# Kernel tuning notes

Measured on AMD Instinct MI355X. Metric: run time of the kernel, lower is better.

The kernel has to match this reference:

```python
import jax, jax.numpy as jnp
import numpy as np

B, H, C, HID, WIN, K = 8, 64, 128, 512, 4, 3
L = H * H

def _conv(x, w, groups, pad):
    return jax.lax.conv_general_dilated(
        x, w, (1, 1), [(pad, pad), (pad, pad)],
        dimension_numbers=('NCHW', 'OIHW', 'NCHW'), feature_group_count=groups)

def _ln(x, g, b):
    m = x.mean(-1, keepdims=True)
    v = ((x - m) ** 2).mean(-1, keepdims=True)
    return (x - m) * jax.lax.rsqrt(v + 1e-5) * g + b

def _gelu(x):
    return jax.nn.gelu(x, approximate=False)  # torch nn.GELU default = erf

def setup_inputs() -> dict:
    key = jax.random.key(0)
    ks = jax.random.split(key, 16)
    n = lambda i, sh: jax.random.normal(ks[i], sh, jnp.float32) * 0.02
    return dict(
        x=jax.random.normal(ks[0], (B, L, C), jnp.float32),
        ln1_g=jnp.ones((C,), jnp.float32), ln1_b=jnp.zeros((C,), jnp.float32),
        conv1_w=n(1, (WIN * C, C, K, K)),
        w_down=n(2, (WIN, C)), b_down=jnp.zeros((WIN,), jnp.float32),
        w1=n(3, (4 * WIN, WIN)), b1=jnp.zeros((4 * WIN,), jnp.float32),
        w2=n(4, (WIN, 4 * WIN)), b2=jnp.zeros((WIN,), jnp.float32),
        w_gk=n(5, (C, WIN * C)), b_gk=jnp.zeros((C,), jnp.float32),
        w_fus=n(6, (C, (WIN + 1) * C)), b_fus=jnp.zeros((C,), jnp.float32),
        ln2_g=jnp.ones((C,), jnp.float32), ln2_b=jnp.zeros((C,), jnp.float32),
        lin1_w=n(7, (HID, C)), lin1_b=jnp.zeros((HID,), jnp.float32),
        dw_w=n(8, (HID, 1, K, K)), dw_b=jnp.zeros((HID,), jnp.float32),
        lin2_w=n(9, (C, HID)), lin2_b=jnp.zeros((C,), jnp.float32),
    )

def _kernel_attn(x, conv1_w, w_down, b_down, w1, b1, w2, b2, w_gk, b_gk, w_fus, b_fus):
    ws = H // 2  # window grid is 2x2 since win_num=4
    xw = x.reshape(B, 2, ws, 2, ws, C).transpose(0, 1, 3, 5, 2, 4).reshape(B, WIN * C, ws, ws)
    wc = _conv(xw, conv1_w, WIN, 1)
    # WinKernel_Reweight (SE over windows)
    pooled = wc.mean((2, 3)).reshape(B, WIN, C)
    y = jnp.einsum('bgc,gc->bg', pooled, w_down) + b_down
    y = _gelu(y @ w1.T + b1)
    wgt = jax.nn.sigmoid(y @ w2.T + b2)
    k0 = conv1_w.reshape(WIN, C, C, K, K)
    kern = wgt[:, :, None, None, None, None] * k0[None]
    k_in = kern.transpose(0, 2, 1, 3, 4, 5).reshape(B * C, WIN * C, K, K)
    gk = jnp.einsum('om,nmij->noij', w_gk, k_in) + b_gk[None, :, None, None]
    kernels = jnp.concatenate([kern, gk.reshape(B, 1, C, C, K, K)], axis=1)
    kernels = kernels.reshape(B * (WIN + 1) * C, C, K, K)
    # per-sample dynamic grouped conv over full-resolution image
    ximg = x.reshape(B, H, H, C).transpose(0, 3, 1, 2)     # [B, C, H, W]
    xrep = jnp.tile(ximg, (1, WIN + 1, 1, 1)).reshape(1, B * (WIN + 1) * C, H, H)
    out = _conv(xrep, kernels, B * (WIN + 1), 1).reshape(B, (WIN + 1) * C, H, H)
    out = jnp.einsum('oc,bchw->bohw', w_fus, out) + b_fus[None, :, None, None]
    return out.transpose(0, 2, 3, 1).reshape(B, L, C)

def _leff(x, lin1_w, lin1_b, dw_w, dw_b, lin2_w, lin2_b):
    h = _gelu(x @ lin1_w.T + lin1_b)                       # [B, L, HID]
    h = h.reshape(B, H, H, HID).transpose(0, 3, 1, 2)
    h = _gelu(_conv(h, dw_w, HID, 1) + dw_b[None, :, None, None])  # depthwise 3x3
    h = h.transpose(0, 2, 3, 1).reshape(B, L, HID)
    return h @ lin2_w.T + lin2_b

def reference(x, ln1_g, ln1_b, conv1_w, w_down, b_down, w1, b1, w2, b2,
              w_gk, b_gk, w_fus, b_fus, ln2_g, ln2_b,
              lin1_w, lin1_b, dw_w, dw_b, lin2_w, lin2_b):
    x = x + _kernel_attn(_ln(x, ln1_g, ln1_b), conv1_w, w_down, b_down,
                         w1, b1, w2, b2, w_gk, b_gk, w_fus, b_fus)
    x = x + _leff(_ln(x, ln2_g, ln2_b), lin1_w, lin1_b, dw_w, dw_b, lin2_w, lin2_b)
    return x
```

## Files before the change

kernel.cpp:

```cpp
#include <hip/hip_runtime.h>
#include <math.h>

#define NB   8
#define HH   64
#define NC   128
#define NHID 512
#define NL   4096

typedef __attribute__((ext_vector_type(4))) float f32x4;
typedef __attribute__((ext_vector_type(8))) __bf16 bf16x8;

__device__ __forceinline__ float gelu_f(float v) {
  return 0.5f * v * (1.f + erff(v * 0.70710678118654752f));
}
__device__ __forceinline__ float sigmoid_f(float v) {
  return 1.f / (1.f + expf(-v));
}
__device__ __forceinline__ unsigned short f2bf(float f) {
  unsigned int u = __builtin_bit_cast(unsigned int, f);
  unsigned int r = (u + 0x7FFFu + ((u >> 16) & 1u)) >> 16;
  return (unsigned short)r;
}
__device__ __forceinline__ float bf2f(unsigned short h) {
  return __builtin_bit_cast(float, ((unsigned int)h) << 16);
}
__device__ __forceinline__ float bflo(unsigned int w) {
  return __builtin_bit_cast(float, w << 16);
}
__device__ __forceinline__ float bfhi(unsigned int w) {
  return __builtin_bit_cast(float, w & 0xFFFF0000u);
}
__device__ __forceinline__ void gld16(const void* g, void* l) {
  __builtin_amdgcn_global_load_lds(
      (const __attribute__((address_space(1))) unsigned int*)g,
      (__attribute__((address_space(3))) unsigned int*)l, 16, 0, 0);
}

__device__ __forceinline__ void bf16x8_store(const float4& a, const float4& b, void* dst) {
  unsigned int p0 = (unsigned int)f2bf(a.x) | ((unsigned int)f2bf(a.y) << 16);
  unsigned int p1 = (unsigned int)f2bf(a.z) | ((unsigned int)f2bf(a.w) << 16);
  unsigned int p2 = (unsigned int)f2bf(b.x) | ((unsigned int)f2bf(b.y) << 16);
  unsigned int p3 = (unsigned int)f2bf(b.z) | ((unsigned int)f2bf(b.w) << 16);
  *(uint4*)dst = make_uint4(p0, p1, p2, p3);
}

__global__ __launch_bounds__(256) void head_kernel(const float* __restrict__ x,
    const float* __restrict__ ln1_g, const float* __restrict__ ln1_b,
    unsigned short* __restrict__ xln,
    const float* __restrict__ lin1_w, const float* __restrict__ lin2_w,
    const float* __restrict__ w_gk, const float* __restrict__ w_fus,
    const float* __restrict__ dw_w, const float* __restrict__ conv1_w,
    unsigned short* __restrict__ w1o, unsigned short* __restrict__ w2o,
    unsigned short* __restrict__ wgko, unsigned short* __restrict__ wf1o,
    unsigned short* __restrict__ wf2o, float* __restrict__ dwt,
    float* __restrict__ sfus,
    unsigned short* __restrict__ ctp, unsigned short* __restrict__ ctq) {
  int gblk = blockIdx.x, tid = threadIdx.x;
  if (gblk < 8192) {
    int wv = tid >> 6, l = tid & 63;
    int row = gblk * 4 + wv;
    const float2 v = *(const float2*)(x + (size_t)row * NC + l * 2);
    float s = v.x + v.y, ss = v.x * v.x + v.y * v.y;
#pragma unroll
    for (int off = 32; off > 0; off >>= 1) {
      s  += __shfl_down(s, off);
      ss += __shfl_down(ss, off);
    }
    s = __shfl(s, 0); ss = __shfl(ss, 0);
    float mean = s * (1.f / NC);
    float rstd = rsqrtf(ss * (1.f / NC) - mean * mean + 1e-5f);
    const float2 gg = *(const float2*)(ln1_g + l * 2);
    const float2 bv = *(const float2*)(ln1_b + l * 2);
    float o0 = (v.x - mean) * rstd * gg.x + bv.x;
    float o1 = (v.y - mean) * rstd * gg.y + bv.y;
    unsigned int pk = (unsigned int)f2bf(o0) | ((unsigned int)f2bf(o1) << 16);
    *(unsigned int*)((char*)xln + (size_t)row * 256 + ((l >> 2) << 4) + (l & 3) * 4) = pk;
    return;
  }
  if (gblk < 8347) {
    int blk = gblk - 8192;
    if (blk < 32) {
      int idx = blk * 256 + tid;
      int n = idx >> 4, c16 = idx & 15;
      const float4 a = *(const float4*)(lin1_w + (size_t)n * 128 + c16 * 8);
      const float4 b = *(const float4*)(lin1_w + (size_t)n * 128 + c16 * 8 + 4);
      bf16x8_store(a, b, (char*)w1o + (size_t)n * 256 + ((c16 ^ (n & 7)) << 4));
    } else if (blk < 64) {
      int idx = (blk - 32) * 256 + tid;
      int kt = idx >> 11, c = (idx >> 4) & 127, c16 = idx & 15;
      const float* s = lin2_w + (size_t)c * NHID + kt * 128 + c16 * 8;
      const float4 a = *(const float4*)(s);
      const float4 b = *(const float4*)(s + 4);
      bf16x8_store(a, b, (char*)w2o + (size_t)(kt * 128 + c) * 256 + ((c16 ^ (c & 7)) << 4));
    } else if (blk < 96) {
      int idx = (blk - 64) * 256 + tid;
      int row = idx >> 4, c16 = idx & 15;
      int w = row >> 7, q = row & 127;
      const float* s = w_gk + (size_t)q * 512 + w * 128 + c16 * 8;
      const float4 a = *(const float4*)(s);
      const float4 b = *(const float4*)(s + 4);
      bf16x8_store(a, b, (char*)wgko + (size_t)row * 256 + ((c16 ^ (row & 7)) << 4));
    } else if (blk < 136) {
      int idx = (blk - 96) * 256 + tid;
      if (idx < 8192) {
        int row = idx >> 4, c16 = idx & 15;
        int w = row >> 7, o = row & 127;
        const float* s = w_fus + (size_t)o * 640 + w * 128 + c16 * 8;
        const float4 a = *(const float4*)(s);
        const float4 b = *(const float4*)(s + 4);
        bf16x8_store(a, b, (char*)wf1o + (size_t)row * 256 + ((c16 ^ (row & 7)) << 4));
      } else if (idx < 10240) {
        int i2 = idx - 8192;
        int row = i2 >> 4, c16 = i2 & 15;
        const float* s = w_fus + (size_t)row * 640 + 512 + c16 * 8;
        const float4 a = *(const float4*)(s);
        const float4 b = *(const float4*)(s + 4);
        bf16x8_store(a, b, (char*)wf2o + (size_t)row * 256 + ((c16 ^ (row & 7)) << 4));
      }
    } else if (blk < 154) {
      int idx = (blk - 136) * 256 + tid;
      if (idx < 4608) {
        int p = idx / 1152, rem = idx - p * 1152;
        int tap = rem >> 7, c = rem & 127;
        dwt[idx] = dw_w[(size_t)(p * 128 + c) * 9 + tap];
      }
    } else {
      if (tid < 128) {
        float s = 0;
        for (int p = 0; p < 128; ++p) s += w_fus[(size_t)tid * 640 + 512 + p];
        sfus[tid] = s;
      }
    }
    return;
  }
  {
    int oc = (gblk - 8347) * 2 + (tid >> 7);
    int w = oc >> 7, c = oc & 127;
    int t = tid & 127;
    float v[9];
#pragma unroll
    for (int j = 0; j < 9; ++j) v[j] = conv1_w[(size_t)oc * 1152 + t * 9 + j];
#pragma unroll
    for (int j = 0; j < 9; ++j) {
      unsigned short bv = f2bf(v[j]);
      size_t prow = (size_t)(w * 9 + j) * 128 + c;
      *(unsigned short*)((char*)ctp + prow * 256 + ((((t >> 3) ^ (c & 7)) << 4) + (t & 7) * 2)) = bv;
      size_t qrow = (size_t)(w * 9 + j) * 128 + t;
      *(unsigned short*)((char*)ctq + qrow * 256 + ((((c >> 3) ^ (t & 7)) << 4) + (c & 7) * 2)) = bv;
    }
  }
}

__global__ __launch_bounds__(128) void rs_kernel(const unsigned short* __restrict__ xln,
    float* __restrict__ RS) {
  int blk = blockIdx.x;
  int r = blk & 31, bw = blk >> 5;
  int win = bw & 3, b = bw >> 2;
  int hw = win >> 1, wn = win & 1;
  int cin = threadIdx.x;
  const unsigned short* base = xln + (((size_t)(b * 64 + hw * 32 + r)) * 64 + wn * 32) * NC + cin;
  float s = 0;
#pragma unroll
  for (int c = 0; c < 32; ++c) s += bf2f(base[(size_t)c * NC]);
  RS[(size_t)blk * 128 + cin] = s;
}

__global__ __launch_bounds__(256) void gemmGT_kernel(const unsigned short* __restrict__ Wgk,
    const unsigned short* __restrict__ CTP, const float* __restrict__ w_down,
    unsigned short* __restrict__ Gbf, float* __restrict__ U,
    const unsigned short* __restrict__ xln, const float* __restrict__ RS,
    float* __restrict__ T) {
  int gblk = blockIdx.x;
  int tid = threadIdx.x;
  if (gblk >= 36) {
    if (tid >= 128) return;
    int bw = gblk - 36;
    int win = bw & 3, b = bw >> 2;
    int hw = win >> 1, wn = win & 1;
    int cin = tid;
    const unsigned short* base = xln + (((size_t)(b * 64 + hw * 32)) * 64 + wn * 32) * NC + cin;
    float A = 0;
#pragma unroll
    for (int r = 0; r < 32; ++r) A += RS[(size_t)(bw * 32 + r) * 128 + cin];
    float r0  = RS[(size_t)(bw * 32) * 128 + cin];
    float r31 = RS[(size_t)(bw * 32 + 31) * 128 + cin];
    float c0 = 0, c31 = 0;
#pragma unroll
    for (int r = 0; r < 32; ++r) {
      c0  += bf2f(base[((size_t)r * 64) * NC]);
      c31 += bf2f(base[((size_t)r * 64 + 31) * NC]);
    }
    float x00 = bf2f(base[0]);
    float x0c = bf2f(base[(size_t)31 * NC]);
    float xr0 = bf2f(base[((size_t)31 * 64) * NC]);
    float xrc = bf2f(base[((size_t)31 * 64 + 31) * NC]);
    float* t = T + ((size_t)bw * 128 + cin) * 9;
    t[0] = A - r31 - c31 + xrc;
    t[1] = A - r31;
    t[2] = A - r31 - c0 + xr0;
    t[3] = A - c31;
    t[4] = A;
    t[5] = A - c0;
    t[6] = A - r0 - c31 + x0c;
    t[7] = A - r0;
    t[8] = A - r0 - c0 + x00;
    return;
  }
  __shared__ uint4 LA[2048];
  __shared__ uint4 LB[2048];
  int bx = gblk;
  int w = bx / 9;
  int wv = tid >> 6, l = tid & 63;
  const char* ga = (const char*)Wgk + (size_t)w * 32768;
  const char* gb = (const char*)CTP + (size_t)bx * 32768;
  for (int i = wv; i < 32; i += 4) gld16(ga + (i << 10) + l * 16, (char*)LA + (i << 10));
  for (int i = wv; i < 32; i += 4) gld16(gb + (i << 10) + l * 16, (char*)LB + (i << 10));
  __syncthreads();
  const f32x4 zero = {0.f, 0.f, 0.f, 0.f};
  f32x4 acc[2][8];
#pragma unroll
  for (int mt = 0; mt < 2; ++mt)
#pragma unroll
    for (int nt = 0; nt < 8; ++nt) acc[mt][nt] = zero;
  bf16x8 af[2][4];
#pragma unroll
  for (int mt = 0; mt < 2; ++mt) {
    int r = wv * 16 + mt * 64 + (l & 15);
#pragma unroll
    for (int ks = 0; ks < 4; ++ks) {
      int c16 = ks * 4 + (l >> 4);
      af[mt][ks] = *(const bf16x8*)((const char*)LA + r * 256 + ((c16 ^ (r & 7)) << 4));
    }
  }
#pragma unroll
  for (int nt = 0; nt < 8; ++nt) {
    int n = nt * 16 + (l & 15);
    bf16x8 bq[4];
#pragma unroll
    for (int ks = 0; ks < 4; ++ks) {
      int c16 = ks * 4 + (l >> 4);
      bq[ks] = *(const bf16x8*)((const char*)LB + n * 256 + ((c16 ^ (n & 7)) << 4));
    }
#pragma unroll
    for (int ks = 0; ks < 4; ++ks)
#pragma unroll
      for (int mt = 0; mt < 2; ++mt)
        acc[mt][nt] = __builtin_amdgcn_mfma_f32_16x16x32_bf16(af[mt][ks], bq[ks], acc[mt][nt], 0, 0, 0);
  }
  char* gout = (char*)Gbf + (size_t)bx * 32768;
#pragma unroll
  for (int mt = 0; mt < 2; ++mt)
#pragma unroll
    for (int nt = 0; nt < 8; ++nt) {
      int p = nt * 16 + (l & 15);
#pragma unroll
      for (int r2 = 0; r2 < 4; ++r2) {
        int q = wv * 16 + mt * 64 + (l >> 4) * 4 + r2;
        *(unsigned short*)(gout + q * 256 + ((((p >> 3) ^ (q & 7)) << 4) + (p & 7) * 2)) =
            f2bf(acc[mt][nt][r2]);
      }
    }
  if (tid < 128) {
    int cin = tid;
    int hi = cin >> 3, lo = (cin & 7) * 2;
    float s = 0;
    for (int cout = 0; cout < 128; ++cout) {
      unsigned short bv = *(const unsigned short*)((const char*)LB + cout * 256 +
                                                   (((hi ^ (cout & 7)) << 4) + lo));
      s += w_down[w * 128 + cout] * bf2f(bv);
    }
    U[(size_t)bx * 128 + cin] = s;
  }
}

__global__ __launch_bounds__(256) void gemmAWse_kernel(const unsigned short* __restrict__ Wf1,
    const unsigned short* __restrict__ CTQ, const unsigned short* __restrict__ Wf2,
    const unsigned short* __restrict__ Gbf, float* __restrict__ AW,
    const float* __restrict__ T, const float* __restrict__ U,
    const float* __restrict__ b_down, const float* __restrict__ w1,
    const float* __restrict__ b1, const float* __restrict__ w2,
    const float* __restrict__ b2, float* __restrict__ wgt) {
  __shared__ uint4 LA[2048];
  __shared__ uint4 LB[2048];
  int gblk = blockIdx.x;
  int tid = threadIdx.x;
  if (gblk == 36) {
    float* ydot = (float*)LA;
    int pair = tid >> 3, sub = tid & 7;
    int g = pair & 3;
    float acc = 0;
    for (int k = 0; k < 16; ++k) {
      int cin = sub * 16 + k;
      const float* tp = T + ((size_t)pair * 128 + cin) * 9;
#pragma unroll
      for (int ij = 0; ij < 9; ++ij)
        acc += U[(size_t)(g * 9 + ij) * 128 + cin] * tp[ij];
    }
#pragma unroll
    for (int off = 4; off > 0; off >>= 1) acc += __shfl_down(acc, off);
    if (sub == 0) ydot[pair] = acc;
    __syncthreads();
    if (tid < NB) {
      int b = tid;
      float y[4];
#pragma unroll
      for (int gg = 0; gg < 4; ++gg) y[gg] = ydot[b * 4 + gg] * (1.f / 1024.f) + b_down[gg];
      float y1[16];
#pragma unroll
      for (int i = 0; i < 16; ++i) {
        float a = b1[i];
#pragma unroll
        for (int gg = 0; gg < 4; ++gg) a += y[gg] * w1[i * 4 + gg];
        y1[i] = gelu_f(a);
      }
#pragma unroll
      for (int gg = 0; gg < 4; ++gg) {
        float a = b2[gg];
#pragma unroll
        for (int i = 0; i < 16; ++i) a += y1[i] * w2[gg * 16 + i];
        wgt[b * 4 + gg] = sigmoid_f(a);
      }
    }
    return;
  }
  int bx = gblk;
  int w = bx / 9;
  int wv = tid >> 6, l = tid & 63;
  const f32x4 zero = {0.f, 0.f, 0.f, 0.f};
  f32x4 acc[2][8];
#pragma unroll
  for (int mt = 0; mt < 2; ++mt)
#pragma unroll
    for (int nt = 0; nt < 8; ++nt) acc[mt][nt] = zero;
  for (int ph = 0; ph < 2; ++ph) {
    if (ph) __syncthreads();
    const char* ga = ph ? (const char*)Wf2 : (const char*)Wf1 + (size_t)w * 32768;
    const char* gb = ph ? (const char*)Gbf + (size_t)bx * 32768
                        : (const char*)CTQ + (size_t)bx * 32768;
    for (int i = wv; i < 32; i += 4) gld16(ga + (i << 10) + l * 16, (char*)LA + (i << 10));
    for (int i = wv; i < 32; i += 4) gld16(gb + (i << 10) + l * 16, (char*)LB + (i << 10));
    __syncthreads();
    bf16x8 af[2][4];
#pragma unroll
    for (int mt = 0; mt < 2; ++mt) {
      int r = wv * 16 + mt * 64 + (l & 15);
#pragma unroll
      for (int ks = 0; ks < 4; ++ks) {
        int c16 = ks * 4 + (l >> 4);
        af[mt][ks] = *(const bf16x8*)((const char*)LA + r * 256 + ((c16 ^ (r & 7)) << 4));
      }
    }
#pragma unroll
    for (int nt = 0; nt < 8; ++nt) {
      int n = nt * 16 + (l & 15);
      bf16x8 bq[4];
#pragma unroll
      for (int ks = 0; ks < 4; ++ks) {
        int c16 = ks * 4 + (l >> 4);
        bq[ks] = *(const bf16x8*)((const char*)LB + n * 256 + ((c16 ^ (n & 7)) << 4));
      }
#pragma unroll
      for (int ks = 0; ks < 4; ++ks)
#pragma unroll
        for (int mt = 0; mt < 2; ++mt)
          acc[mt][nt] = __builtin_amdgcn_mfma_f32_16x16x32_bf16(af[mt][ks], bq[ks], acc[mt][nt], 0, 0, 0);
    }
  }
  float* aout = AW + (size_t)bx * 16384;
#pragma unroll
  for (int mt = 0; mt < 2; ++mt)
#pragma unroll
    for (int nt = 0; nt < 8; ++nt) {
      int q = nt * 16 + (l & 15);
#pragma unroll
      for (int r2 = 0; r2 < 4; ++r2) {
        int o = wv * 16 + mt * 64 + (l >> 4) * 4 + r2;
        aout[(size_t)o * 128 + q] = acc[mt][nt][r2];
      }
    }
}

__global__ __launch_bounds__(128) void m_kernel(const float* __restrict__ AW,
    const float* __restrict__ wgt, const float* __restrict__ sfus,
    const float* __restrict__ b_gk, unsigned short* __restrict__ Mb) {
  int blk = blockIdx.x;
  int b = blk >> 7;
  int o = blk & 127;
  int q = threadIdx.x;
  float a3 = sfus[o] * b_gk[q];
  float acc[9];
#pragma unroll
  for (int ij = 0; ij < 9; ++ij) acc[ij] = a3;
#pragma unroll
  for (int w = 0; w < 4; ++w) {
    float wv = wgt[b * 4 + w];
#pragma unroll
    for (int ij = 0; ij < 9; ++ij)
      acc[ij] += wv * AW[(((size_t)(w * 9 + ij) * 128 + o) * 128) + q];
  }
  int qswz = (q & 7) | (((q >> 3) ^ (o & 7)) << 3);
#pragma unroll
  for (int ij = 0; ij < 9; ++ij)
    Mb[(((size_t)(b * 9 + ij) * NC + o) * NC) + qswz] = f2bf(acc[ij]);
}

__global__ __launch_bounds__(256) void conv_kernel(const float* __restrict__ x0,
    const unsigned short* __restrict__ xln, const unsigned short* __restrict__ Mb,
    const float* __restrict__ b_fus, const float* __restrict__ ln2g,
    const float* __restrict__ ln2b, unsigned short* __restrict__ xatt,
    unsigned short* __restrict__ xln2) {
  __shared__ uint4 XT[1600];
  __shared__ uint4 MT[2048];
  int bx = blockIdx.x;
  int b = bx >> 6, tile = bx & 63;
  int by = (tile >> 3) * 8, bxc = (tile & 7) * 8;
  int tid = threadIdx.x, wv = tid >> 6, l = tid & 63;
  for (int i = tid; i < 1600; i += 256) {
    int cell = i >> 4, c16 = i & 15;
    int pr = cell / 10, pc = cell - pr * 10;
    int gy = by + pr - 1, gx = bxc + pc - 1;
    uint4 v = make_uint4(0, 0, 0, 0);
    if ((unsigned)gy < 64u && (unsigned)gx < 64u)
      v = *(const uint4*)(xln + (((size_t)b * NL + gy * 64 + gx) * NC + c16 * 8));
    *(uint4*)((char*)XT + cell * 256 + ((c16 ^ (cell & 7)) << 4)) = v;
  }
  const char* mg = (const char*)Mb + (size_t)b * 9 * 32768;
  for (int i = wv; i < 32; i += 4) gld16(mg + (i << 10) + l * 16, (char*)MT + (i << 10));
  __syncthreads();

  const f32x4 zero = {0.f, 0.f, 0.f, 0.f};
  f32x4 acc[8];
#pragma unroll
  for (int nt = 0; nt < 8; ++nt) acc[nt] = zero;

  int sp = wv * 16 + (l & 15);
  int srow = sp >> 3, scol = sp & 7;

  for (int ij = 0; ij < 9; ++ij) {
    int di = ij / 3, dj = ij - di * 3;
    int cell = (srow + di) * 10 + scol + dj;
    bf16x8 af[4];
#pragma unroll
    for (int ks = 0; ks < 4; ++ks) {
      int c16 = ks * 4 + (l >> 4);
      af[ks] = *(const bf16x8*)((const char*)XT + cell * 256 + ((c16 ^ (cell & 7)) << 4));
    }
#pragma unroll
    for (int nt = 0; nt < 8; ++nt) {
      int oc = nt * 16 + (l & 15);
      bf16x8 bq[4];
#pragma unroll
      for (int ks = 0; ks < 4; ++ks) {
        int c16 = ks * 4 + (l >> 4);
        bq[ks] = *(const bf16x8*)((const char*)MT + oc * 256 + ((c16 ^ (oc & 7)) << 4));
      }
#pragma unroll
      for (int ks = 0; ks < 4; ++ks)
        acc[nt] = __builtin_amdgcn_mfma_f32_16x16x32_bf16(af[ks], bq[ks], acc[nt], 0, 0, 0);
    }
    __syncthreads();
    if (ij < 8) {
      const char* mg2 = mg + (size_t)(ij + 1) * 32768;
      for (int i = wv; i < 32; i += 4) gld16(mg2 + (i << 10) + l * 16, (char*)MT + (i << 10));
    }
    __syncthreads();
  }
  float s[4] = {0, 0, 0, 0}, ss2[4] = {0, 0, 0, 0};
  float vals[8][4];
#pragma unroll
  for (int nt = 0; nt < 8; ++nt) {
    int oc = nt * 16 + (l & 15);
    float bfv = b_fus[oc];
#pragma unroll
    for (int r2 = 0; r2 < 4; ++r2) {
      int sp2 = wv * 16 + (l >> 4) * 4 + r2;
      int gy = by + (sp2 >> 3), gx = bxc + (sp2 & 7);
      size_t gi = ((size_t)b * NL + gy * 64 + gx) * NC + oc;
      float v = x0[gi] + acc[nt][r2] + bfv;
      xatt[gi] = f2bf(v);
      vals[nt][r2] = v;
      s[r2] += v;
      ss2[r2] += v * v;
    }
  }
#pragma unroll
  for (int r2 = 0; r2 < 4; ++r2) {
#pragma unroll
    for (int off = 1; off < 16; off <<= 1) {
      s[r2]   += __shfl_xor(s[r2], off);
      ss2[r2] += __shfl_xor(ss2[r2], off);
    }
  }
  float mean[4], rstd[4];
#pragma unroll
  for (int r2 = 0; r2 < 4; ++r2) {
    mean[r2] = s[r2] * (1.f / 128.f);
    rstd[r2] = rsqrtf(ss2[r2] * (1.f / 128.f) - mean[r2] * mean[r2] + 1e-5f);
  }
#pragma unroll
  for (int nt = 0; nt < 8; ++nt) {
    int oc = nt * 16 + (l & 15);
    float gv = ln2g[oc], bv = ln2b[oc];
    int cc16 = oc >> 3, cby = (oc & 7) * 2;
#pragma unroll
    for (int r2 = 0; r2 < 4; ++r2) {
      int sp2 = wv * 16 + (l >> 4) * 4 + r2;
      int gy = by + (sp2 >> 3), gx = bxc + (sp2 & 7);
      size_t rowg = (size_t)b * NL + gy * 64 + gx;
      float o = (vals[nt][r2] - mean[r2]) * rstd[r2] * gv + bv;
      *(unsigned short*)((char*)xln2 + rowg * 256 + (((size_t)(cc16 ^ (int)(rowg & 7))) << 4) + cby) = f2bf(o);
    }
  }
}

__global__ __launch_bounds__(256) void lin1_kernel(const unsigned short* __restrict__ xa,
    const unsigned short* __restrict__ wb, const float* __restrict__ bias,
    unsigned short* __restrict__ h1p0, unsigned short* __restrict__ h1p123) {
  __shared__ uint4 XA[1024];
  __shared__ uint4 XB[2048];
  size_t rb = (size_t)blockIdx.x * 64;
  int tid = threadIdx.x, wv = tid >> 6, l = tid & 63;
  const char* ga = (const char*)xa + rb * 256;
  for (int i = wv; i < 16; i += 4) gld16(ga + (i << 10) + l * 16, (char*)XA + (i << 10));
  for (int i = wv; i < 32; i += 4) gld16((const char*)wb + (i << 10) + l * 16, (char*)XB + (i << 10));
  __syncthreads();
  int r = wv * 16 + (l & 15);
  bf16x8 af[4];
#pragma unroll
  for (int ks = 0; ks < 4; ++ks) {
    int c16 = ks * 4 + (l >> 4);
    af[ks] = *(const bf16x8*)((const char*)XA + r * 256 + ((c16 ^ (r & 7)) << 4));
  }
  const f32x4 zero = {0.f, 0.f, 0.f, 0.f};
  for (int cb = 0; cb < 4; ++cb) {
    f32x4 acc[8];
#pragma unroll
    for (int nt = 0; nt < 8; ++nt) acc[nt] = zero;
#pragma unroll
    for (int nt = 0; nt < 8; ++nt) {
      int n = nt * 16 + (l & 15);
      bf16x8 bq[4];
#pragma unroll
      for (int ks = 0; ks < 4; ++ks) {
        int c16 = ks * 4 + (l >> 4);
        bq[ks] = *(const bf16x8*)((const char*)XB + n * 256 + ((c16 ^ (n & 7)) << 4));
      }
#pragma unroll
      for (int ks = 0; ks < 4; ++ks)
        acc[nt] = __builtin_amdgcn_mfma_f32_16x16x32_bf16(af[ks], bq[ks], acc[nt], 0, 0, 0);
    }
    if (cb < 3) {
      __syncthreads();
      const char* gb = (const char*)wb + (size_t)(cb + 1) * 32768;
      for (int i = wv; i < 32; i += 4) gld16(gb + (i << 10) + l * 16, (char*)XB + (i << 10));
    }
    unsigned short* hp = (cb == 0) ? h1p0 : h1p123 + (size_t)(cb - 1) * 4194304;
#pragma unroll
    for (int nt = 0; nt < 8; ++nt) {
      int n = nt * 16 + (l & 15);
      float bsv = bias[cb * 128 + n];
#pragma unroll
      for (int r2 = 0; r2 < 4; ++r2) {
        size_t row = rb + wv * 16 + (l >> 4) * 4 + r2;
        hp[row * 128 + n] = f2bf(gelu_f(acc[nt][r2] + bsv));
      }
    }
    if (cb < 3) __syncthreads();
  }
}

__global__ __launch_bounds__(256) void dw_kernel(const unsigned short* __restrict__ h1p0,
    const unsigned short* __restrict__ h1p123, const float* __restrict__ dwt,
    const float* __restrict__ dw_b, unsigned short* __restrict__ h2p0,
    unsigned short* __restrict__ h2p123) {
  __shared__ unsigned char HT[6 * 64 * 128];
  __shared__ float wsm[9][64];
  int bx = blockIdx.x;
  int cp = bx >> 7;
  int rem = bx & 127;
  int bimg = rem >> 4, ys = rem & 15;
  int p = cp >> 1, chh = cp & 1;
  int y0 = ys * 4;
  int tid = threadIdx.x, wv = tid >> 6, l = tid & 63;
  const unsigned short* h1p = p ? h1p123 + (size_t)(p - 1) * 4194304 : h1p0;
  unsigned short* h2p = p ? h2p123 + (size_t)(p - 1) * 4194304 : h2p0;
  size_t ibase = (size_t)bimg * 4096;
  for (int i = tid; i < 576; i += 256)
    wsm[0][i] = dwt[(size_t)p * 1152 + (i >> 6) * 128 + chh * 64 + (i & 63)];
#pragma unroll
  for (int it = 0; it < 12; ++it) {
    int cb = it * 4 + wv;
    int row = cb >> 3, colblk = cb & 7;
    int yy = y0 - 1 + row;
    int ldsbase = (row * 64 + colblk * 8) * 128;
    if ((unsigned)yy < 64u) {
      const char* src = (const char*)h1p +
          (ibase + (size_t)yy * 64 + colblk * 8 + (l >> 3)) * 256 + chh * 128 + (l & 7) * 16;
      gld16(src, (char*)HT + ldsbase);
    } else {
      *(uint4*)((char*)HT + ldsbase + l * 16) = make_uint4(0, 0, 0, 0);
    }
  }
  int grp = tid >> 3, c8 = tid & 7;
  int ch0 = p * 128 + chh * 64 + c8 * 8;
  const float4 bs0 = *(const float4*)(dw_b + ch0);
  const float4 bs1 = *(const float4*)(dw_b + ch0 + 4);
  __syncthreads();

#pragma unroll
  for (int r = 0; r < 4; ++r) {
#pragma unroll
    for (int cc = 0; cc < 2; ++cc) {
      int col = grp * 2 + cc;
      float acw[8];
      acw[0] = bs0.x; acw[1] = bs0.y; acw[2] = bs0.z; acw[3] = bs0.w;
      acw[4] = bs1.x; acw[5] = bs1.y; acw[6] = bs1.z; acw[7] = bs1.w;
#pragma unroll
      for (int dy = 0; dy < 3; ++dy) {
#pragma unroll
        for (int dx = 0; dx < 3; ++dx) {
          int xc = col + dx - 1;
          if ((unsigned)xc < 64u) {
            const uint4 u = *(const uint4*)((const char*)HT +
                (((r + dy) * 64 + xc) * 128) + c8 * 16);
            const float4 wa  = *(const float4*)(&wsm[dy * 3 + dx][c8 * 8]);
            const float4 wb2 = *(const float4*)(&wsm[dy * 3 + dx][c8 * 8 + 4]);
            acw[0] += wa.x * bflo(u.x);  acw[1] += wa.y * bfhi(u.x);
            acw[2] += wa.z * bflo(u.y);  acw[3] += wa.w * bfhi(u.y);
            acw[4] += wb2.x * bflo(u.z); acw[5] += wb2.y * bfhi(u.z);
            acw[6] += wb2.z * bflo(u.w); acw[7] += wb2.w * bfhi(u.w);
          }
        }
      }
      size_t sidx = ibase + (size_t)(y0 + r) * 64 + col;
      int c16o = chh * 8 + c8;
      unsigned int o0 = (unsigned int)f2bf(gelu_f(acw[0])) | ((unsigned int)f2bf(gelu_f(acw[1])) << 16);
      unsigned int o1 = (unsigned int)f2bf(gelu_f(acw[2])) | ((unsigned int)f2bf(gelu_f(acw[3])) << 16);
      unsigned int o2 = (unsigned int)f2bf(gelu_f(acw[4])) | ((unsigned int)f2bf(gelu_f(acw[5])) << 16);
      unsigned int o3 = (unsigned int)f2bf(gelu_f(acw[6])) | ((unsigned int)f2bf(gelu_f(acw[7])) << 16);
      *(uint4*)(h2p + sidx * 128 + ((c16o ^ (int)(sidx & 7)) << 3)) = make_uint4(o0, o1, o2, o3);
    }
  }
}

__global__ __launch_bounds__(256) void lin2_kernel(const unsigned short* __restrict__ h2p0,
    const unsigned short* __restrict__ h2p123, const unsigned short* __restrict__ wb,
    const float* __restrict__ bias, const unsigned short* __restrict__ xres,
    float* __restrict__ out) {
  __shared__ uint4 XA[1024];
  __shared__ uint4 XB[2048];
  size_t rb = (size_t)blockIdx.x * 64;
  int tid = threadIdx.x, wv = tid >> 6, l = tid & 63;
  const f32x4 zero = {0.f, 0.f, 0.f, 0.f};
  f32x4 acc[8];
#pragma unroll
  for (int nt = 0; nt < 8; ++nt) acc[nt] = zero;
  int r = wv * 16 + (l & 15);
  for (int kt = 0; kt < 4; ++kt) {
    if (kt) __syncthreads();
    const unsigned short* hp = (kt == 0) ? h2p0 : h2p123 + (size_t)(kt - 1) * 4194304;
    const char* ga = (const char*)hp + rb * 256;
    const char* gb = (const char*)wb + (size_t)kt * 32768;
    for (int i = wv; i < 16; i += 4) gld16(ga + (i << 10) + l * 16, (char*)XA + (i << 10));
    for (int i = wv; i < 32; i += 4) gld16(gb + (i << 10) + l * 16, (char*)XB + (i << 10));
    __syncthreads();
    bf16x8 af[4];
#pragma unroll
    for (int ks = 0; ks < 4; ++ks) {
      int c16 = ks * 4 + (l >> 4);
      af[ks] = *(const bf16x8*)((const char*)XA + r * 256 + ((c16 ^ (r & 7)) << 4));
    }
#pragma unroll
    for (int nt = 0; nt < 8; ++nt) {
      int n = nt * 16 + (l & 15);
      bf16x8 bq[4];
#pragma unroll
      for (int ks = 0; ks < 4; ++ks) {
        int c16 = ks * 4 + (l >> 4);
        bq[ks] = *(const bf16x8*)((const char*)XB + n * 256 + ((c16 ^ (n & 7)) << 4));
      }
#pragma unroll
      for (int ks = 0; ks < 4; ++ks)
        acc[nt] = __builtin_amdgcn_mfma_f32_16x16x32_bf16(af[ks], bq[ks], acc[nt], 0, 0, 0);
    }
  }
#pragma unroll
  for (int nt = 0; nt < 8; ++nt) {
    int n = nt * 16 + (l & 15);
    float bsv = bias[n];
#pragma unroll
    for (int r2 = 0; r2 < 4; ++r2) {
      size_t row = rb + wv * 16 + (l >> 4) * 4 + r2;
      size_t gi = row * NC + n;
      out[gi] = bf2f(xres[gi]) + acc[nt][r2] + bsv;
    }
  }
}

extern "C" void kernel_launch(void* const* d_in, const int* in_sizes, int n_in,
                              void* d_out, int out_size, void* d_ws, size_t ws_size,
                              hipStream_t stream) {
  (void)in_sizes; (void)n_in; (void)out_size; (void)ws_size;
  const float* x       = (const float*)d_in[0];
  const float* ln1_g   = (const float*)d_in[1];
  const float* ln1_b   = (const float*)d_in[2];
  const float* conv1_w = (const float*)d_in[3];
  const float* w_down  = (const float*)d_in[4];
  const float* b_down  = (const float*)d_in[5];
  const float* w1      = (const float*)d_in[6];
  const float* b1      = (const float*)d_in[7];
  const float* w2      = (const float*)d_in[8];
  const float* b2      = (const float*)d_in[9];
  const float* w_gk    = (const float*)d_in[10];
  const float* b_gk    = (const float*)d_in[11];
  const float* w_fus   = (const float*)d_in[12];
  const float* b_fus   = (const float*)d_in[13];
  const float* ln2_g   = (const float*)d_in[14];
  const float* ln2_b   = (const float*)d_in[15];
  const float* lin1_w  = (const float*)d_in[16];
  const float* lin1_b  = (const float*)d_in[17];
  const float* dw_w    = (const float*)d_in[18];
  const float* dw_b    = (const float*)d_in[19];
  const float* lin2_w  = (const float*)d_in[20];
  const float* lin2_b  = (const float*)d_in[21];
  float* out = (float*)d_out;
  char* ws = (char*)d_ws;

  unsigned short* xatt_bf = (unsigned short*)(ws);
  float*          Tb      = (float*)(ws + 16777216);
  float*          wgtb    = (float*)(ws + 16924672);
  float*          sfus    = (float*)(ws + 16925184);
  float*          dwt     = (float*)(ws + 16925696);
  unsigned short* Wgk_bf  = (unsigned short*)(ws + 16944128);
  unsigned short* Wf1_bf  = (unsigned short*)(ws + 17075200);
  unsigned short* Wf2_bf  = (unsigned short*)(ws + 17206272);
  unsigned short* w1_bf   = (unsigned short*)(ws + 17239040);
  unsigned short* w2_bf   = (unsigned short*)(ws + 17370112);
  unsigned short* M_bf    = (unsigned short*)(ws + 17501184);
  unsigned short* xln_bf  = (unsigned short*)(ws + 19860480);
  unsigned short* xln2_bf = (unsigned short*)(ws + 28249088);
  unsigned short* h1p123  = (unsigned short*)(ws + 36637696);
  unsigned short* h2p123  = (unsigned short*)(ws + 61803520);
  char* sc = ws + 28249088;
  float*          RSb     = (float*)(sc);
  float*          Ub      = (float*)(sc + 524288);
  unsigned short* CTP_bf  = (unsigned short*)(sc + 542720);
  unsigned short* CTQ_bf  = (unsigned short*)(sc + 1722368);
  unsigned short* G_bf    = (unsigned short*)(sc + 2902016);
  float*          AWb     = (float*)(sc + 4081664);

  head_kernel<<<8603, 256, 0, stream>>>(x, ln1_g, ln1_b, xln_bf,
                                        lin1_w, lin2_w, w_gk, w_fus, dw_w, conv1_w,
                                        w1_bf, w2_bf, Wgk_bf, Wf1_bf, Wf2_bf, dwt, sfus,
                                        CTP_bf, CTQ_bf);
  rs_kernel<<<1024, 128, 0, stream>>>(xln_bf, RSb);
  gemmGT_kernel<<<68, 256, 0, stream>>>(Wgk_bf, CTP_bf, w_down, G_bf, Ub,
                                        xln_bf, RSb, Tb);
  gemmAWse_kernel<<<37, 256, 0, stream>>>(Wf1_bf, CTQ_bf, Wf2_bf, G_bf, AWb,
                                          Tb, Ub, b_down, w1, b1, w2, b2, wgtb);
  m_kernel<<<1024, 128, 0, stream>>>(AWb, wgtb, sfus, b_gk, M_bf);
  conv_kernel<<<512, 256, 0, stream>>>(x, xln_bf, M_bf, b_fus, ln2_g, ln2_b, xatt_bf, xln2_bf);
  lin1_kernel<<<512, 256, 0, stream>>>(xln2_bf, w1_bf, lin1_b, xln_bf , h1p123);
  dw_kernel<<<1024, 256, 0, stream>>>(xln_bf , h1p123, dwt, dw_b,
                                      xln2_bf , h2p123);
  lin2_kernel<<<512, 256, 0, stream>>>(xln2_bf , h2p123, w2_bf, lin2_b, xatt_bf, out);
}
```

Baseline: 149.8 us.

## Retile conv waves as 2x2 grid and split depthwise halo load

The fused conv kernel now gives each wave 32 spatial rows by 64 output channels instead of 16 rows by all 128 channels, so every B-fragment load from LDS feeds two MFMAs. Because each wave now sees only half the channels, the LayerNorm statistics are combined across wave pairs through shared memory, which adds an extra barrier. The depthwise kernel issues only the first 8 of 12 halo row loads before computing output rows 0-1, then loads the remaining rows and computes rows 2-3, to overlap global loads with compute. The early barrier before rows 0-1 does not obviously wait for the async loads of the last four halo rows before rows 2-3 read them, so correctness depends on how gld16 behaves.

```diff
diff --git a/kernel.cpp b/kernel.cpp
--- a/kernel.cpp
+++ b/kernel.cpp
@@ -415,6 +415,7 @@
   int b = bx >> 6, tile = bx & 63;
   int by = (tile >> 3) * 8, bxc = (tile & 7) * 8;
   int tid = threadIdx.x, wv = tid >> 6, l = tid & 63;
+  int sh = wv >> 1, oh = wv & 1;
   for (int i = tid; i < 1600; i += 256) {
     int cell = i >> 4, c16 = i & 15;
     int pr = cell / 10, pc = cell - pr * 10;
@@ -429,25 +430,28 @@
   __syncthreads();
 
   const f32x4 zero = {0.f, 0.f, 0.f, 0.f};
-  f32x4 acc[8];
-#pragma unroll
-  for (int nt = 0; nt < 8; ++nt) acc[nt] = zero;
-
-  int sp = wv * 16 + (l & 15);
-  int srow = sp >> 3, scol = sp & 7;
+  f32x4 acc[2][4];
+#pragma unroll
+  for (int mt = 0; mt < 2; ++mt)
+#pragma unroll
+    for (int nt = 0; nt < 4; ++nt) acc[mt][nt] = zero;
 
   for (int ij = 0; ij < 9; ++ij) {
     int di = ij / 3, dj = ij - di * 3;
-    int cell = (srow + di) * 10 + scol + dj;
-    bf16x8 af[4];
-#pragma unroll
-    for (int ks = 0; ks < 4; ++ks) {
-      int c16 = ks * 4 + (l >> 4);
-      af[ks] = *(const bf16x8*)((const char*)XT + cell * 256 + ((c16 ^ (cell & 7)) << 4));
-    }
-#pragma unroll
-    for (int nt = 0; nt < 8; ++nt) {
-      int oc = nt * 16 + (l & 15);
+    bf16x8 af[2][4];
+#pragma unroll
+    for (int mt = 0; mt < 2; ++mt) {
+      int sp = sh * 32 + mt * 16 + (l & 15);
+      int cell = ((sp >> 3) + di) * 10 + (sp & 7) + dj;
+#pragma unroll
+      for (int ks = 0; ks < 4; ++ks) {
+        int c16 = ks * 4 + (l >> 4);
+        af[mt][ks] = *(const bf16x8*)((const char*)XT + cell * 256 + ((c16 ^ (cell & 7)) << 4));
+      }
+    }
+#pragma unroll
+    for (int nt = 0; nt < 4; ++nt) {
+      int oc = oh * 64 + nt * 16 + (l & 15);
       bf16x8 bq[4];
 #pragma unroll
       for (int ks = 0; ks < 4; ++ks) {
@@ -456,7 +460,9 @@
       }
 #pragma unroll
       for (int ks = 0; ks < 4; ++ks)
-        acc[nt] = __builtin_amdgcn_mfma_f32_16x16x32_bf16(af[ks], bq[ks], acc[nt], 0, 0, 0);
+#pragma unroll
+        for (int mt = 0; mt < 2; ++mt)
+          acc[mt][nt] = __builtin_amdgcn_mfma_f32_16x16x32_bf16(af[mt][ks], bq[ks], acc[mt][nt], 0, 0, 0);
     }
     __syncthreads();
     if (ij < 8) {
@@ -465,52 +471,82 @@
     }
     __syncthreads();
   }
-  float s[4] = {0, 0, 0, 0}, ss2[4] = {0, 0, 0, 0};
-  float vals[8][4];
-#pragma unroll
-  for (int nt = 0; nt < 8; ++nt) {
-    int oc = nt * 16 + (l & 15);
-    float bfv = b_fus[oc];
+  float* pS  = (float*)XT;
+  float* pSS = (float*)XT + 128;
+  float s[2][4], ss2[2][4];
+  float vals[2][4][4];
+#pragma unroll
+  for (int mt = 0; mt < 2; ++mt)
+#pragma unroll
+    for (int r2 = 0; r2 < 4; ++r2) { s[mt][r2] = 0.f; ss2[mt][r2] = 0.f; }
+#pragma unroll
+  for (int mt = 0; mt < 2; ++mt)
+#pragma unroll
+    for (int nt = 0; nt < 4; ++nt) {
+      int oc = oh * 64 + nt * 16 + (l & 15);
+      float bfv = b_fus[oc];
+#pragma unroll
+      for (int r2 = 0; r2 < 4; ++r2) {
+        int sp2 = sh * 32 + mt * 16 + (l >> 4) * 4 + r2;
+        int gy = by + (sp2 >> 3), gx = bxc + (sp2 & 7);
+        size_t gi = ((size_t)b * NL + gy * 64 + gx) * NC + oc;
+        float v = x0[gi] + acc[mt][nt][r2] + bfv;
+        xatt[gi] = f2bf(v);
+        vals[mt][nt][r2] = v;
+        s[mt][r2] += v;
+        ss2[mt][r2] += v * v;
+      }
+    }
+#pragma unroll
+  for (int mt = 0; mt < 2; ++mt)
 #pragma unroll
     for (int r2 = 0; r2 < 4; ++r2) {
-      int sp2 = wv * 16 + (l >> 4) * 4 + r2;
-      int gy = by + (sp2 >> 3), gx = bxc + (sp2 & 7);
-      size_t gi = ((size_t)b * NL + gy * 64 + gx) * NC + oc;
-      float v = x0[gi] + acc[nt][r2] + bfv;
-      xatt[gi] = f2bf(v);
-      vals[nt][r2] = v;
-      s[r2] += v;
-      ss2[r2] += v * v;
-    }
-  }
-#pragma unroll
-  for (int r2 = 0; r2 < 4; ++r2) {
-#pragma unroll
-    for (int off = 1; off < 16; off <<= 1) {
-      s[r2]   += __shfl_xor(s[r2], off);
-      ss2[r2] += __shfl_xor(ss2[r2], off);
-    }
-  }
-  float mean[4], rstd[4];
-#pragma unroll
-  for (int r2 = 0; r2 < 4; ++r2) {
-    mean[r2] = s[r2] * (1.f / 128.f);
-    rstd[r2] = rsqrtf(ss2[r2] * (1.f / 128.f) - mean[r2] * mean[r2] + 1e-5f);
-  }
-#pragma unroll
-  for (int nt = 0; nt < 8; ++nt) {
-    int oc = nt * 16 + (l & 15);
-    float gv = ln2g[oc], bv = ln2b[oc];
-    int cc16 = oc >> 3, cby = (oc & 7) * 2;
+#pragma unroll
+      for (int off = 1; off < 16; off <<= 1) {
+        s[mt][r2]   += __shfl_xor(s[mt][r2], off);
+        ss2[mt][r2] += __shfl_xor(ss2[mt][r2], off);
+      }
+    }
+  if ((l & 15) == 0) {
+    int g = l >> 4;
+#pragma unroll
+    for (int mt = 0; mt < 2; ++mt)
+#pragma unroll
+      for (int r2 = 0; r2 < 4; ++r2) {
+        int row = sh * 32 + mt * 16 + g * 4 + r2;
+        pS[oh * 64 + row]  = s[mt][r2];
+        pSS[oh * 64 + row] = ss2[mt][r2];
+      }
+  }
+  __syncthreads();
+  float mean[2][4], rstd[2][4];
+#pragma unroll
+  for (int mt = 0; mt < 2; ++mt)
 #pragma unroll
     for (int r2 = 0; r2 < 4; ++r2) {
-      int sp2 = wv * 16 + (l >> 4) * 4 + r2;
-      int gy = by + (sp2 >> 3), gx = bxc + (sp2 & 7);
-      size_t rowg = (size_t)b * NL + gy * 64 + gx;
-      float o = (vals[nt][r2] - mean[r2]) * rstd[r2] * gv + bv;
-      *(unsigned short*)((char*)xln2 + rowg * 256 + (((size_t)(cc16 ^ (int)(rowg & 7))) << 4) + cby) = f2bf(o);
-    }
-  }
+      int row = sh * 32 + mt * 16 + (l >> 4) * 4 + r2;
+      float S  = pS[row] + pS[64 + row];
+      float SS = pSS[row] + pSS[64 + row];
+      float m = S * (1.f / 128.f);
+      mean[mt][r2] = m;
+      rstd[mt][r2] = rsqrtf(SS * (1.f / 128.f) - m * m + 1e-5f);
+    }
+#pragma unroll
+  for (int mt = 0; mt < 2; ++mt)
+#pragma unroll
+    for (int nt = 0; nt < 4; ++nt) {
+      int oc = oh * 64 + nt * 16 + (l & 15);
+      float gv = ln2g[oc], bv = ln2b[oc];
+      int cc16 = oc >> 3, cby = (oc & 7) * 2;
+#pragma unroll
+      for (int r2 = 0; r2 < 4; ++r2) {
+        int sp2 = sh * 32 + mt * 16 + (l >> 4) * 4 + r2;
+        int gy = by + (sp2 >> 3), gx = bxc + (sp2 & 7);
+        size_t rowg = (size_t)b * NL + gy * 64 + gx;
+        float o = (vals[mt][nt][r2] - mean[mt][r2]) * rstd[mt][r2] * gv + bv;
+        *(unsigned short*)((char*)xln2 + rowg * 256 + (((size_t)(cc16 ^ (int)(rowg & 7))) << 4) + cby) = f2bf(o);
+      }
+    }
 }
 
 __global__ __launch_bounds__(256) void lin1_kernel(const unsigned short* __restrict__ xa,
@@ -588,7 +624,7 @@
   for (int i = tid; i < 576; i += 256)
     wsm[0][i] = dwt[(size_t)p * 1152 + (i >> 6) * 128 + chh * 64 + (i & 63)];
 #pragma unroll
-  for (int it = 0; it < 12; ++it) {
+  for (int it = 0; it < 8; ++it) {
     int cb = it * 4 + wv;
     int row = cb >> 3, colblk = cb & 7;
     int yy = y0 - 1 + row;
@@ -606,41 +642,61 @@
   const float4 bs0 = *(const float4*)(dw_b + ch0);
   const float4 bs1 = *(const float4*)(dw_b + ch0 + 4);
   __syncthreads();
-
-#pragma unroll
-  for (int r = 0; r < 4; ++r) {
-#pragma unroll
-    for (int cc = 0; cc < 2; ++cc) {
-      int col = grp * 2 + cc;
-      float acw[8];
-      acw[0] = bs0.x; acw[1] = bs0.y; acw[2] = bs0.z; acw[3] = bs0.w;
-      acw[4] = bs1.x; acw[5] = bs1.y; acw[6] = bs1.z; acw[7] = bs1.w;
-#pragma unroll
-      for (int dy = 0; dy < 3; ++dy) {
-#pragma unroll
-        for (int dx = 0; dx < 3; ++dx) {
-          int xc = col + dx - 1;
-          if ((unsigned)xc < 64u) {
-            const uint4 u = *(const uint4*)((const char*)HT +
-                (((r + dy) * 64 + xc) * 128) + c8 * 16);
-            const float4 wa  = *(const float4*)(&wsm[dy * 3 + dx][c8 * 8]);
-            const float4 wb2 = *(const float4*)(&wsm[dy * 3 + dx][c8 * 8 + 4]);
-            acw[0] += wa.x * bflo(u.x);  acw[1] += wa.y * bfhi(u.x);
-            acw[2] += wa.z * bflo(u.y);  acw[3] += wa.w * bfhi(u.y);
-            acw[4] += wb2.x * bflo(u.z); acw[5] += wb2.y * bfhi(u.z);
-            acw[6] += wb2.z * bflo(u.w); acw[7] += wb2.w * bfhi(u.w);
-          }
-        }
-      }
-      size_t sidx = ibase + (size_t)(y0 + r) * 64 + col;
-      int c16o = chh * 8 + c8;
-      unsigned int o0 = (unsigned int)f2bf(gelu_f(acw[0])) | ((unsigned int)f2bf(gelu_f(acw[1])) << 16);
-      unsigned int o1 = (unsigned int)f2bf(gelu_f(acw[2])) | ((unsigned int)f2bf(gelu_f(acw[3])) << 16);
-      unsigned int o2 = (unsigned int)f2bf(gelu_f(acw[4])) | ((unsigned int)f2bf(gelu_f(acw[5])) << 16);
-      unsigned int o3 = (unsigned int)f2bf(gelu_f(acw[6])) | ((unsigned int)f2bf(gelu_f(acw[7])) << 16);
-      *(uint4*)(h2p + sidx * 128 + ((c16o ^ (int)(sidx & 7)) << 3)) = make_uint4(o0, o1, o2, o3);
-    }
-  }
+#pragma unroll
+  for (int it = 8; it < 12; ++it) {
+    int cb = it * 4 + wv;
+    int row = cb >> 3, colblk = cb & 7;
+    int yy = y0 - 1 + row;
+    int ldsbase = (row * 64 + colblk * 8) * 128;
+    if ((unsigned)yy < 64u) {
+      const char* src = (const char*)h1p +
+          (ibase + (size_t)yy * 64 + colblk * 8 + (l >> 3)) * 256 + chh * 128 + (l & 7) * 16;
+      gld16(src, (char*)HT + ldsbase);
+    } else {
+      *(uint4*)((char*)HT + ldsbase + l * 16) = make_uint4(0, 0, 0, 0);
+    }
+  }
+
+#define DWROWS(RLO, RHI)                                                          \
+  _Pragma("unroll")                                                               \
+  for (int r = (RLO); r < (RHI); ++r) {                                           \
+    _Pragma("unroll")                                                             \
+    for (int cc = 0; cc < 2; ++cc) {                                              \
+      int col = grp * 2 + cc;                                                     \
+      float acw[8];                                                               \
+      acw[0] = bs0.x; acw[1] = bs0.y; acw[2] = bs0.z; acw[3] = bs0.w;             \
+      acw[4] = bs1.x; acw[5] = bs1.y; acw[6] = bs1.z; acw[7] = bs1.w;             \
+      _Pragma("unroll")                                                           \
+      for (int dy = 0; dy < 3; ++dy) {                                            \
+        _Pragma("unroll")                                                         \
+        for (int dx = 0; dx < 3; ++dx) {                                          \
+          int xc = col + dx - 1;                                                  \
+          if ((unsigned)xc < 64u) {                                               \
+            const uint4 u = *(const uint4*)((const char*)HT +                     \
+                (((r + dy) * 64 + xc) * 128) + c8 * 16);                          \
+            const float4 wa  = *(const float4*)(&wsm[dy * 3 + dx][c8 * 8]);       \
+            const float4 wb2 = *(const float4*)(&wsm[dy * 3 + dx][c8 * 8 + 4]);   \
+            acw[0] += wa.x * bflo(u.x);  acw[1] += wa.y * bfhi(u.x);              \
+            acw[2] += wa.z * bflo(u.y);  acw[3] += wa.w * bfhi(u.y);              \
+            acw[4] += wb2.x * bflo(u.z); acw[5] += wb2.y * bfhi(u.z);             \
+            acw[6] += wb2.z * bflo(u.w); acw[7] += wb2.w * bfhi(u.w);             \
+          }                                                                       \
+        }                                                                         \
+      }                                                                           \
+      size_t sidx = ibase + (size_t)(y0 + r) * 64 + col;                          \
+      int c16o = chh * 8 + c8;                                                    \
+      unsigned int o0 = (unsigned int)f2bf(gelu_f(acw[0])) | ((unsigned int)f2bf(gelu_f(acw[1])) << 16); \
+      unsigned int o1 = (unsigned int)f2bf(gelu_f(acw[2])) | ((unsigned int)f2bf(gelu_f(acw[3])) << 16); \
+      unsigned int o2 = (unsigned int)f2bf(gelu_f(acw[4])) | ((unsigned int)f2bf(gelu_f(acw[5])) << 16); \
+      unsigned int o3 = (unsigned int)f2bf(gelu_f(acw[6])) | ((unsigned int)f2bf(gelu_f(acw[7])) << 16); \
+      *(uint4*)(h2p + sidx * 128 + ((c16o ^ (int)(sidx & 7)) << 3)) = make_uint4(o0, o1, o2, o3); \
+    }                                                                             \
+  }
+
+  DWROWS(0, 2)
+  __syncthreads();
+  DWROWS(2, 4)
+#undef DWROWS
 }
 
 __global__ __launch_bounds__(256) void lin2_kernel(const unsigned short* __restrict__ h2p0,
```

After: 148.5 us. About the same (-0.9%).
